# Kernel tuning notes

Measured on AMD Instinct MI355X. Metric: run time of the kernel, lower is better.

Reference implementation:

```python
import jax, jax.numpy as jnp
import numpy as np
from jax.scipy.special import logsumexp

TEMPERATURE = 0.1
BETA = 0.999
EPS = 1e-8
HARD_K = 10  # min(num_classes // 4, 10) with num_classes = 1000


def _l2norm(x, axis=-1):
    return x * jax.lax.rsqrt(jnp.sum(x * x, axis=axis, keepdims=True) + 1e-24)


def setup_inputs() -> dict:
    key = jax.random.key(0)
    k1, k2, k3, k4, k5 = jax.random.split(key, 5)
    B, D, C, M = 4096, 1024, 1000, 32768
    return {
        "image_features": jax.random.normal(k1, (B, D), dtype=jnp.float32),
        "prompts": jax.random.normal(k2, (C, D), dtype=jnp.float32),
        "labels": jax.random.randint(k3, (B, C), 0, 2, dtype=jnp.int32),
        "memory_features": jax.random.normal(k4, (M, D), dtype=jnp.float32),
        "memory_labels": jax.random.randint(k5, (M, C), 0, 2, dtype=jnp.int32),
        "mem_ptr": 16384,
    }


def reference(image_features, prompts, labels, memory_features, memory_labels, mem_ptr):
    B, D = image_features.shape
    C = prompts.shape[0]
    labels_f = labels.astype(jnp.float32)

    # z_img = F.normalize(image_features)
    z_img = _l2norm(image_features, axis=1)

    # class weights (effective-number reweighting), computed from this batch's labels
    counts = labels_f.sum(axis=0)                              # [C]
    effective_num = 1.0 - jnp.power(jnp.float32(BETA), counts)
    weights = (1.0 - BETA) / (effective_num + EPS)
    weights = weights / jnp.sum(weights) * C                   # [C]

    # memory bank update (detached write of current batch at ptr), then use [:ptr+B]
    mem_f = memory_features.at[mem_ptr:mem_ptr + B].set(jax.lax.stop_gradient(z_img))
    mem_l = memory_labels.at[mem_ptr:mem_ptr + B].set(labels)
    used = mem_ptr + B  # static

    enhanced_features = jnp.concatenate([z_img, mem_f[:used]], axis=0)     # [N, D]
    enhanced_labels = jnp.concatenate([labels_f, mem_l[:used].astype(jnp.float32)], axis=0)  # [N, C]

    z_prompts = _l2norm(prompts, axis=1)                       # [C, D]
    sim = (enhanced_features @ z_prompts.T) / TEMPERATURE      # [N, C]

    pos_mask = enhanced_labels > 0                             # [N, C]

    # hard negatives: top-K similarities among negatives define the keep threshold
    sim_for_neg = jnp.where(pos_mask, -jnp.inf, sim)
    hard_neg_vals, _ = jax.lax.top_k(sim_for_neg, HARD_K)      # [N, K]
    min_hard_neg = hard_neg_vals[:, -1:]                       # [N, 1]
    neg_mask = (~pos_mask) & (sim >= min_hard_neg)
    full_mask = pos_mask | neg_mask

    lse = logsumexp(jnp.where(full_mask, sim, -jnp.inf), axis=1)  # [N]
    log_prob = sim - lse[:, None]                              # [N, C]

    posf = pos_mask.astype(sim.dtype)
    pos_w = posf * weights[None, :]                            # [N, C]
    weight_sums = pos_w.sum(axis=1)                            # [N]
    loss_num = (pos_w * (-log_prob)).sum(axis=1)               # [N]

    valid = weight_sums > 0
    loss_per_sample = jnp.where(valid, loss_num / (weight_sums + EPS), 0.0)
    n_valid = jnp.maximum(valid.sum(), 1)
    attr_loss = loss_per_sample.sum() / n_valid.astype(sim.dtype)
    # single attribute -> total_loss / num_valid_attrs == attr_loss
    return attr_loss
```

## Files before the change

kernel.cpp:

```cpp
#include <hip/hip_runtime.h>
#include <math.h>

#define BN    4096
#define DD    1024
#define CC    1000
#define MM    32768
#define ROWS_CAP 32768


#define NGROUP_A 512
#define NGROUP_B 16
#define NCOUNT   512
#define NBITS    512

#define NSUB 16

typedef __attribute__((ext_vector_type(8))) int   int8v;
typedef __attribute__((ext_vector_type(16))) float f32x16;

__device__ __forceinline__ float wave_sum_f(float v) {
#pragma unroll
  for (int off = 32; off >= 1; off >>= 1) v += __shfl_xor(v, off, 64);
  return v;
}

__device__ __forceinline__ int pack4(float a, float b, float c, float d) {
  int p = __builtin_amdgcn_cvt_pk_fp8_f32(a, b, 0, false);
  p = __builtin_amdgcn_cvt_pk_fp8_f32(c, d, p, true);
  return p;
}

__device__ __forceinline__ void gload16(const unsigned char* g, unsigned char* l) {
  __builtin_amdgcn_global_load_lds(
      (const __attribute__((address_space(1))) unsigned int*)g,
      (__attribute__((address_space(3))) unsigned int*)l, 16, 0, 0);
}

__device__ __forceinline__ void ins10(float* t, float v) {
#pragma unroll
  for (int i = 9; i >= 1; --i) t[i] = __builtin_amdgcn_fmed3f(v, t[i - 1], t[i]);
  t[0] = fmaxf(t[0], v);
}

__global__ __launch_bounds__(256) void conv_kernel(const float* __restrict__ img,
                                                   const float* __restrict__ prompts,
                                                   const float* __restrict__ mem,
                                                   const int* __restrict__ memptr,
                                                   unsigned char* __restrict__ A,
                                                   unsigned char* __restrict__ B,
                                                   const int* __restrict__ labels,
                                                   const int* __restrict__ mlabels,
                                                   int* __restrict__ counts,
                                                   unsigned* __restrict__ bitmask) {
  const int blk = blockIdx.x;
  const int t = threadIdx.x;
  const int lane = t & 63;
  const int wid = t >> 6;
  const int nrows = BN + memptr[0];
  const int padded = (nrows + 127) & ~127;

  if (blk >= NGROUP_A + NGROUP_B + NCOUNT) {
    const int bi = blk - (NGROUP_A + NGROUP_B + NCOUNT);
    const int rowBase = bi * 64;
    if (rowBase >= padded) return;
    for (int i = 0; i < 16; ++i) {
      const int row = rowBase + wid * 16 + i;
      if (row >= padded) continue;
      unsigned bits = 0;
      if (row < nrows) {
        const int* lr = (row < BN) ? labels + (size_t)row * CC
                                   : mlabels + (size_t)(row - BN) * CC;
        const int cbase = lane * 16;
#pragma unroll
        for (int g = 0; g < 4; ++g) {
          int c = cbase + g * 4;
          int4 l4;
          if (c + 3 < CC) l4 = *(const int4*)(lr + c);
          else {
            l4.x = (c < CC) ? lr[c] : 0;
            l4.y = (c + 1 < CC) ? lr[c + 1] : 0;
            l4.z = (c + 2 < CC) ? lr[c + 2] : 0;
            l4.w = (c + 3 < CC) ? lr[c + 3] : 0;
          }
          unsigned m = 0;
          if (l4.x > 0) m |= 1u;
          if (l4.y > 0) m |= 2u;
          if (l4.z > 0) m |= 4u;
          if (l4.w > 0) m |= 8u;
          bits |= m << (g * 4);
        }
      }
      unsigned pair = __shfl_xor(bits, 1, 64);
      if (!(lane & 1)) bitmask[(size_t)row * 32 + (lane >> 1)] = bits | (pair << 16);
    }
    return;
  }

  if (blk >= NGROUP_A + NGROUP_B) {
    const int ci = blk - (NGROUP_A + NGROUP_B);
    const int c = (ci & 3) * 256 + t;
    if (c >= CC) return;
    const int b0 = (ci >> 2) * 32;
    int s = 0;
#pragma unroll
    for (int b = 0; b < 32; ++b) s += labels[(size_t)(b0 + b) * CC + c];
    atomicAdd(&counts[c], s);
    return;
  }

  __shared__ unsigned char tile[65536];

  const bool isB = (blk >= NGROUP_A);
  const int g = isB ? (blk - NGROUP_A) : blk;
  const int rowBase = g * 64;
  if (!isB && rowBase >= padded) return;

  unsigned char* dstBase = (isB ? B : A)
      + (size_t)(rowBase >> 7) * 131072 + (size_t)(rowBase & 64) * 16;

  for (int i = 0; i < 16; ++i) {
    const int r = wid * 16 + i;
    const int row = rowBase + r;
    const float* src = nullptr;
    float esc = 1.0f;
    bool needNorm = false;
    if (isB) {
      if (row < CC) { src = prompts + (size_t)row * DD; needNorm = true; esc = 10.0f; }
    } else {
      if (row < BN)         { src = img + (size_t)row * DD; needNorm = true; }
      else if (row < nrows) { src = mem + (size_t)(row - BN) * DD; }
    }
    int4 o = {0, 0, 0, 0};
    if (src) {
      const float4* s4 = (const float4*)src + lane * 4;
      float4 a = s4[0], b = s4[1], c = s4[2], d = s4[3];
      float sc = esc;
      if (needNorm) {
        float ss = a.x * a.x + a.y * a.y + a.z * a.z + a.w * a.w
                 + b.x * b.x + b.y * b.y + b.z * b.z + b.w * b.w
                 + c.x * c.x + c.y * c.y + c.z * c.z + c.w * c.w
                 + d.x * d.x + d.y * d.y + d.z * d.z + d.w * d.w;
        ss = wave_sum_f(ss);
        sc = esc * rsqrtf(ss + 1e-24f);
      }
      o.x = pack4(a.x * sc, a.y * sc, a.z * sc, a.w * sc);
      o.y = pack4(b.x * sc, b.y * sc, b.z * sc, b.w * sc);
      o.z = pack4(c.x * sc, c.y * sc, c.z * sc, c.w * sc);
      o.w = pack4(d.x * sc, d.y * sc, d.z * sc, d.w * sc);
    }
    *(int4*)(tile + lane * 1024 + (((r + lane) & 63) << 4)) = o;
  }
  __syncthreads();

#pragma unroll
  for (int p = 0; p < 16; ++p) {
    const int ochunk = p * 256 + t;
    const int kc = ochunk >> 6;
    const int rl = ochunk & 63;
    int4 v = *(const int4*)(tile + kc * 1024 + (((rl + kc) & 63) << 4));
    *(int4*)(dstBase + (size_t)kc * 2048 + rl * 16) = v;
  }
}

__global__ __launch_bounds__(512) void gemm_fused(
    const unsigned char* __restrict__ A, const unsigned char* __restrict__ Bm,
    const unsigned* __restrict__ bitmask, const int* __restrict__ counts,
    const int* __restrict__ memptr, float* __restrict__ partials) {
  const int f = blockIdx.x;
  const int x = f & 7;
  const int s = f >> 3;
  const int cb = s & 7;
  const int rt = (s >> 3) * 8 + x;

  const int nrows = BN + memptr[0];
  const int row0 = rt * 128;
  if (row0 >= nrows) return;
  const int c0 = cb * 128;

  __shared__ unsigned char As[2][16384];
  __shared__ unsigned char Bs[2][16384];
  __shared__ unsigned posbits[128][4];
  __shared__ float wcol[128];
  __shared__ float wpart[8];

  const int t = threadIdx.x;
  const int lane = t & 63;
  const int wid = t >> 6;
  const int wm = (wid >> 1) * 32;
  const int wn = (wid & 1) * 64;
  const int q = lane >> 5;
  const int rr = lane & 31;

  const unsigned char* gaT = A + (size_t)row0 * DD;
  const unsigned char* gbT = Bm + (size_t)c0 * DD;

#pragma unroll
  for (int p = 0; p < 2; ++p) {
    gload16(gaT + p * 8192 + t * 16, As[0] + p * 8192 + t * 16);
    gload16(gbT + p * 8192 + t * 16, Bs[0] + p * 8192 + t * 16);
  }
#pragma unroll
  for (int p = 0; p < 2; ++p) {
    gload16(gaT + 16384 + p * 8192 + t * 16, As[1] + p * 8192 + t * 16);
    gload16(gbT + 16384 + p * 8192 + t * 16, Bs[1] + p * 8192 + t * 16);
  }

  {
    float wv[2];
    float accw = 0.f;
#pragma unroll
    for (int i = 0; i < 2; ++i) {
      int c = t + i * 512;
      float w = 0.f;
      if (c < CC) {
        float cnt = (float)counts[c];
        float en = 1.0f - expf(cnt * logf(0.999f));
        w = (1.0f - 0.999f) / (en + 1e-8f);
      }
      wv[i] = w;
      accw += w;
    }
    float sw = wave_sum_f(accw);
    if (lane == 0) wpart[wid] = sw;
    if (t < 128) {
      const int4 bm = *(const int4*)(bitmask + (size_t)(row0 + t) * 32 + cb * 4);
      posbits[t][0] = bm.x; posbits[t][1] = bm.y;
      posbits[t][2] = bm.z; posbits[t][3] = bm.w;
    }
    __syncthreads();
    float tot = 0.f;
#pragma unroll
    for (int i = 0; i < 8; ++i) tot += wpart[i];
    float scw = (float)CC / tot;
#pragma unroll
    for (int i = 0; i < 2; ++i) {
      int c = t + i * 512;
      if (c >= c0 && c < c0 + 128) wcol[c - c0] = wv[i] * scw;
    }
  }

  f32x16 acc[2] = {};

  int cur = 0;
  for (int it = 0; it < 8; ++it) {
    if (it == 7) asm volatile("s_waitcnt vmcnt(0)" ::: "memory");
    else         asm volatile("s_waitcnt vmcnt(4)" ::: "memory");
    __builtin_amdgcn_sched_barrier(0);
    __builtin_amdgcn_s_barrier();
    __builtin_amdgcn_sched_barrier(0);
#pragma unroll
    for (int h = 0; h < 2; ++h) {
      const int kc = h * 4 + q * 2;
      int8v af, bfv[2];
      {
        const unsigned char* pa = As[cur] + kc * 2048 + (wm + rr) * 16;
        int4 lo4 = *(const int4*)pa;
        int4 hi4 = *(const int4*)(pa + 2048);
        af[0] = lo4.x; af[1] = lo4.y; af[2] = lo4.z; af[3] = lo4.w;
        af[4] = hi4.x; af[5] = hi4.y; af[6] = hi4.z; af[7] = hi4.w;
      }
#pragma unroll
      for (int ni = 0; ni < 2; ++ni) {
        const unsigned char* pb = Bs[cur] + kc * 2048 + (wn + ni * 32 + rr) * 16;
        int4 lo4 = *(const int4*)pb;
        int4 hi4 = *(const int4*)(pb + 2048);
        bfv[ni][0] = lo4.x; bfv[ni][1] = lo4.y; bfv[ni][2] = lo4.z; bfv[ni][3] = lo4.w;
        bfv[ni][4] = hi4.x; bfv[ni][5] = hi4.y; bfv[ni][6] = hi4.z; bfv[ni][7] = hi4.w;
      }
#pragma unroll
      for (int ni = 0; ni < 2; ++ni)
        acc[ni] = __builtin_amdgcn_mfma_scale_f32_32x32x64_f8f6f4(
            bfv[ni], af, acc[ni], 0, 0, 0, 127, 0, 127);
    }
    __builtin_amdgcn_sched_barrier(0);
    __builtin_amdgcn_s_barrier();
    __builtin_amdgcn_sched_barrier(0);
    if (it + 2 < 8) {
      const size_t kb = (size_t)(it + 2) * 16384;
#pragma unroll
      for (int p = 0; p < 2; ++p) {
        gload16(gaT + kb + p * 8192 + t * 16, As[cur] + p * 8192 + t * 16);
        gload16(gbT + kb + p * 8192 + t * 16, Bs[cur] + p * 8192 + t * 16);
      }
    }
    cur ^= 1;
  }

  const int cl = lane & 31;
  const int rl = wm + cl;
  const int row_g = row0 + rl;
  const int wnb = wid & 1;

  float t10[10];
#pragma unroll
  for (int i = 0; i < 10; ++i) t10[i] = -INFINITY;
  float m = -INFINITY, ssum = 0.f, wsum = 0.f, wsim = 0.f;
#pragma unroll
  for (int ni = 0; ni < 2; ++ni) {
    const unsigned bits = posbits[rl][wnb * 2 + ni];
    f32x16 v = acc[ni];
    float pq = -INFINITY;
    unsigned pb = 0;
#pragma unroll
    for (int reg = 0; reg < 16; ++reg) {
      const int ci = (reg & 3) + 8 * (reg >> 2) + 4 * q;
      const int cg = c0 + wn + ni * 32 + ci;
      const float val = v[reg];
      const bool cvalid = (cg < CC);
      const bool pos = cvalid && ((bits >> ci) & 1u);
      if (pos) {
        float w = wcol[wn + ni * 32 + ci];
        wsum += w;
        wsim += w * val;
        pq = fmaxf(pq, val);
        pb |= 1u << reg;
      }
      ins10(t10, (cvalid && !pos) ? val : -INFINITY);
    }
    if (pb) {
      float ps = 0.f;
#pragma unroll
      for (int reg = 0; reg < 16; ++reg)
        ps += expf(((pb >> reg) & 1u) ? (v[reg] - pq) : -INFINITY);
      float m2 = fmaxf(m, pq);
      ssum = ssum * expf(m - m2) + ps * expf(pq - m2);
      m = m2;
    }
  }

  {
    float o10[10];
#pragma unroll
    for (int j = 0; j < 10; ++j) o10[j] = __shfl_xor(t10[j], 32, 64);
#pragma unroll
    for (int j = 0; j < 10; ++j) ins10(t10, o10[j]);
    float pm2 = __shfl_xor(m, 32, 64);
    float ps2 = __shfl_xor(ssum, 32, 64);
    float w2  = __shfl_xor(wsum, 32, 64);
    float ws2 = __shfl_xor(wsim, 32, 64);
    if (ps2 > 0.f) {
      float m2 = fmaxf(m, pm2);
      ssum = ssum * expf(m - m2) + ps2 * expf(pm2 - m2);
      m = m2;
    }
    wsum += w2;
    wsim += ws2;
  }

  if (q == 0) {
    const int sub = cb * 2 + wnb;
    float* pp = partials + (size_t)sub * ROWS_CAP + row_g;
#pragma unroll
    for (int k = 0; k < 10; ++k) pp[(size_t)k * NSUB * ROWS_CAP] = t10[k];
    pp[(size_t)10 * NSUB * ROWS_CAP] = m;
    pp[(size_t)11 * NSUB * ROWS_CAP] = ssum;
    pp[(size_t)12 * NSUB * ROWS_CAP] = wsum;
    pp[(size_t)13 * NSUB * ROWS_CAP] = wsim;
  }
}

__global__ __launch_bounds__(256) void merge_kernel(const float* __restrict__ partials,
                                                    const int* __restrict__ memptr,
                                                    float* __restrict__ blk_lps,
                                                    float* __restrict__ blk_val) {
  const int t = threadIdx.x;
  const int row = blockIdx.x * 256 + t;
  const int nrows = BN + memptr[0];

  float cl = 0.f, cv = 0.f;
  if (row < nrows) {
    float t10[10];
#pragma unroll
    for (int i = 0; i < 10; ++i) t10[i] = -INFINITY;
    float Mp = -INFINITY, psum = 0.f, wsum = 0.f, wsim = 0.f;
    for (int sub = 0; sub < NSUB; ++sub) {
      const float* pp = partials + (size_t)sub * ROWS_CAP + row;
#pragma unroll
      for (int j = 0; j < 10; ++j) ins10(t10, pp[(size_t)j * NSUB * ROWS_CAP]);
      float pm = pp[(size_t)10 * NSUB * ROWS_CAP];
      float ps = pp[(size_t)11 * NSUB * ROWS_CAP];
      wsum += pp[(size_t)12 * NSUB * ROWS_CAP];
      wsim += pp[(size_t)13 * NSUB * ROWS_CAP];
      if (ps > 0.f) {
        float m2 = fmaxf(Mp, pm);
        psum = psum * expf(Mp - m2) + ps * expf(pm - m2);
        Mp = m2;
      }
    }
    const float M = fmaxf(Mp, t10[0]);
    float esum = 0.f;
#pragma unroll
    for (int j = 0; j < 10; ++j) esum += expf(t10[j] - M);
    if (psum > 0.f) esum += psum * expf(Mp - M);
    const float lse = M + logf(esum);
    const bool valid = (wsum > 0.f);
    const float lps = valid ? (wsum * lse - wsim) / (wsum + 1e-8f) : 0.f;
    const float mult = (row < BN) ? 2.f : 1.f;
    cl = mult * lps;
    cv = valid ? mult : 0.f;
  }
  cl = wave_sum_f(cl);
  cv = wave_sum_f(cv);
  __shared__ float p1[4], p2[4];
  if ((t & 63) == 0) { p1[t >> 6] = cl; p2[t >> 6] = cv; }
  __syncthreads();
  if (t == 0) {
    blk_lps[blockIdx.x] = p1[0] + p1[1] + p1[2] + p1[3];
    blk_val[blockIdx.x] = p2[0] + p2[1] + p2[2] + p2[3];
  }
}

__global__ __launch_bounds__(128) void reduce_kernel(const float* __restrict__ blk_lps,
                                                     const float* __restrict__ blk_val,
                                                     float* __restrict__ out) {
  const int t = threadIdx.x;
  float a = wave_sum_f(blk_lps[t]);
  float b = wave_sum_f(blk_val[t]);
  __shared__ float p1[2], p2[2];
  if ((t & 63) == 0) { p1[t >> 6] = a; p2[t >> 6] = b; }
  __syncthreads();
  if (t == 0) out[0] = (p1[0] + p1[1]) / fmaxf(p2[0] + p2[1], 1.0f);
}

extern "C" void kernel_launch(void* const* d_in, const int* in_sizes, int n_in,
                              void* d_out, int out_size, void* d_ws, size_t ws_size,
                              hipStream_t stream) {
  const float* img     = (const float*)d_in[0];
  const float* prompts = (const float*)d_in[1];
  const int*   labels  = (const int*)d_in[2];
  const float* mem     = (const float*)d_in[3];
  const int*   mlabels = (const int*)d_in[4];
  const int*   memptr  = (const int*)d_in[5];
  float* out = (float*)d_out;
  char* ws = (char*)d_ws;

  int*      counts  = (int*)(ws + 0);
  float*    blk_lps = (float*)(ws + 8192);
  float*    blk_val = (float*)(ws + 12288);
  unsigned* bitmask = (unsigned*)(ws + 270336);
  unsigned char* Bf8 = (unsigned char*)(ws + 4464640);
  unsigned char* Af8 = (unsigned char*)(ws + 5513216);
  float* partials = (float*)(ws + 5513216 + (size_t)ROWS_CAP * DD);

  hipMemsetAsync(ws, 0, 4096, stream);

  conv_kernel<<<NGROUP_A + NGROUP_B + NCOUNT + NBITS, 256, 0, stream>>>(
      img, prompts, mem, memptr, Af8, Bf8, labels, mlabels, counts, bitmask);

  gemm_fused<<<8 * (ROWS_CAP / 128), 512, 0, stream>>>(
      Af8, Bf8, bitmask, counts, memptr, partials);

  merge_kernel<<<ROWS_CAP / 256, 256, 0, stream>>>(partials, memptr, blk_lps, blk_val);

  reduce_kernel<<<1, 128, 0, stream>>>(blk_lps, blk_val, out);
}
```

Before: 397.7 us.

## Load GEMM A operand straight to registers and widen conversion blocks to 512 threads

The GEMM kernel no longer stages the A tile in LDS. Each wave loads its A fragments from global memory into registers and prefetches the next k-step, while B keeps a double-buffered LDS prefetch that now runs one step ahead, with a single __syncthreads per iteration. This cuts LDS traffic and shared-memory footprint, aiming for better occupancy or less LDS contention. In exchange, waves that share the same A rows load them redundantly, and the barrier's memory wait may limit how much the loads overlap with compute. The conversion, label-count and bitmask kernels are also regridded to 512-thread blocks with fewer rows per wave and unrolled loops.

```diff
diff --git a/kernel.cpp b/kernel.cpp
--- a/kernel.cpp
+++ b/kernel.cpp
@@ -8,10 +8,10 @@
 #define ROWS_CAP 32768
 
 
-#define NGROUP_A 512
-#define NGROUP_B 16
-#define NCOUNT   512
-#define NBITS    512
+#define NGA   512
+#define NGB   16
+#define NCNT  128
+#define NBIT  1024
 
 #define NSUB 16
 
@@ -42,7 +42,7 @@
   t[0] = fmaxf(t[0], v);
 }
 
-__global__ __launch_bounds__(256) void conv_kernel(const float* __restrict__ img,
+__global__ __launch_bounds__(512) void conv_kernel(const float* __restrict__ img,
                                                    const float* __restrict__ prompts,
                                                    const float* __restrict__ mem,
                                                    const int* __restrict__ memptr,
@@ -59,12 +59,13 @@
   const int nrows = BN + memptr[0];
   const int padded = (nrows + 127) & ~127;
 
-  if (blk >= NGROUP_A + NGROUP_B + NCOUNT) {
-    const int bi = blk - (NGROUP_A + NGROUP_B + NCOUNT);
-    const int rowBase = bi * 64;
+  if (blk >= NGA + NGB + NCNT) {
+    const int bi = blk - (NGA + NGB + NCNT);
+    const int rowBase = bi * 32;
     if (rowBase >= padded) return;
-    for (int i = 0; i < 16; ++i) {
-      const int row = rowBase + wid * 16 + i;
+#pragma unroll
+    for (int i = 0; i < 4; ++i) {
+      const int row = rowBase + wid * 4 + i;
       if (row >= padded) continue;
       unsigned bits = 0;
       if (row < nrows) {
@@ -96,30 +97,35 @@
     return;
   }
 
-  if (blk >= NGROUP_A + NGROUP_B) {
-    const int ci = blk - (NGROUP_A + NGROUP_B);
-    const int c = (ci & 3) * 256 + t;
-    if (c >= CC) return;
-    const int b0 = (ci >> 2) * 32;
-    int s = 0;
-#pragma unroll
-    for (int b = 0; b < 32; ++b) s += labels[(size_t)(b0 + b) * CC + c];
-    atomicAdd(&counts[c], s);
+  if (blk >= NGA + NGB) {
+    const int ci = blk - (NGA + NGB);
+    const int b0 = ci * 32;
+    int s1 = 0, s2 = 0;
+    const bool c2ok = (t + 512 < CC);
+#pragma unroll
+    for (int b = 0; b < 32; ++b) {
+      const int* lr = labels + (size_t)(b0 + b) * CC;
+      s1 += lr[t];
+      if (c2ok) s2 += lr[t + 512];
+    }
+    atomicAdd(&counts[t], s1);
+    if (c2ok) atomicAdd(&counts[t + 512], s2);
     return;
   }
 
   __shared__ unsigned char tile[65536];
 
-  const bool isB = (blk >= NGROUP_A);
-  const int g = isB ? (blk - NGROUP_A) : blk;
+  const bool isB = (blk >= NGA);
+  const int g = isB ? (blk - NGA) : blk;
   const int rowBase = g * 64;
   if (!isB && rowBase >= padded) return;
 
   unsigned char* dstBase = (isB ? B : A)
       + (size_t)(rowBase >> 7) * 131072 + (size_t)(rowBase & 64) * 16;
 
-  for (int i = 0; i < 16; ++i) {
-    const int r = wid * 16 + i;
+#pragma unroll
+  for (int i = 0; i < 8; ++i) {
+    const int r = wid * 8 + i;
     const int row = rowBase + r;
     const float* src = nullptr;
     float esc = 1.0f;
@@ -153,8 +159,8 @@
   __syncthreads();
 
 #pragma unroll
-  for (int p = 0; p < 16; ++p) {
-    const int ochunk = p * 256 + t;
+  for (int p = 0; p < 8; ++p) {
+    const int ochunk = p * 512 + t;
     const int kc = ochunk >> 6;
     const int rl = ochunk & 63;
     int4 v = *(const int4*)(tile + kc * 1024 + (((rl + kc) & 63) << 4));
@@ -177,7 +183,6 @@
   if (row0 >= nrows) return;
   const int c0 = cb * 128;
 
-  __shared__ unsigned char As[2][16384];
   __shared__ unsigned char Bs[2][16384];
   __shared__ unsigned posbits[128][4];
   __shared__ float wcol[128];
@@ -193,17 +198,18 @@
 
   const unsigned char* gaT = A + (size_t)row0 * DD;
   const unsigned char* gbT = Bm + (size_t)c0 * DD;
-
-#pragma unroll
-  for (int p = 0; p < 2; ++p) {
-    gload16(gaT + p * 8192 + t * 16, As[0] + p * 8192 + t * 16);
+  const unsigned char* aBase = gaT + (size_t)(q * 2) * 2048 + (size_t)(wm + rr) * 16;
+
+#pragma unroll
+  for (int p = 0; p < 2; ++p)
     gload16(gbT + p * 8192 + t * 16, Bs[0] + p * 8192 + t * 16);
-  }
-#pragma unroll
-  for (int p = 0; p < 2; ++p) {
-    gload16(gaT + 16384 + p * 8192 + t * 16, As[1] + p * 8192 + t * 16);
-    gload16(gbT + 16384 + p * 8192 + t * 16, Bs[1] + p * 8192 + t * 16);
-  }
+  int4 afc[4], afn[4];
+  afc[0] = *(const int4*)(aBase);
+  afc[1] = *(const int4*)(aBase + 2048);
+  afc[2] = *(const int4*)(aBase + 8192);
+  afc[3] = *(const int4*)(aBase + 8192 + 2048);
+#pragma unroll
+  for (int i = 0; i < 4; ++i) afn[i] = afc[i];
 
   {
     float wv[2];
@@ -243,46 +249,39 @@
 
   int cur = 0;
   for (int it = 0; it < 8; ++it) {
-    if (it == 7) asm volatile("s_waitcnt vmcnt(0)" ::: "memory");
-    else         asm volatile("s_waitcnt vmcnt(4)" ::: "memory");
-    __builtin_amdgcn_sched_barrier(0);
-    __builtin_amdgcn_s_barrier();
-    __builtin_amdgcn_sched_barrier(0);
+    if (it < 7) {
+      const size_t kb = (size_t)(it + 1) * 16384;
+#pragma unroll
+      for (int p = 0; p < 2; ++p)
+        gload16(gbT + kb + p * 8192 + t * 16, Bs[cur ^ 1] + p * 8192 + t * 16);
+      const unsigned char* an = aBase + kb;
+      afn[0] = *(const int4*)(an);
+      afn[1] = *(const int4*)(an + 2048);
+      afn[2] = *(const int4*)(an + 8192);
+      afn[3] = *(const int4*)(an + 8192 + 2048);
+    }
 #pragma unroll
     for (int h = 0; h < 2; ++h) {
       const int kc = h * 4 + q * 2;
-      int8v af, bfv[2];
-      {
-        const unsigned char* pa = As[cur] + kc * 2048 + (wm + rr) * 16;
-        int4 lo4 = *(const int4*)pa;
-        int4 hi4 = *(const int4*)(pa + 2048);
-        af[0] = lo4.x; af[1] = lo4.y; af[2] = lo4.z; af[3] = lo4.w;
-        af[4] = hi4.x; af[5] = hi4.y; af[6] = hi4.z; af[7] = hi4.w;
-      }
+      int8v a, bfv;
+      a[0] = afc[h * 2].x;     a[1] = afc[h * 2].y;
+      a[2] = afc[h * 2].z;     a[3] = afc[h * 2].w;
+      a[4] = afc[h * 2 + 1].x; a[5] = afc[h * 2 + 1].y;
+      a[6] = afc[h * 2 + 1].z; a[7] = afc[h * 2 + 1].w;
 #pragma unroll
       for (int ni = 0; ni < 2; ++ni) {
         const unsigned char* pb = Bs[cur] + kc * 2048 + (wn + ni * 32 + rr) * 16;
         int4 lo4 = *(const int4*)pb;
         int4 hi4 = *(const int4*)(pb + 2048);
-        bfv[ni][0] = lo4.x; bfv[ni][1] = lo4.y; bfv[ni][2] = lo4.z; bfv[ni][3] = lo4.w;
-        bfv[ni][4] = hi4.x; bfv[ni][5] = hi4.y; bfv[ni][6] = hi4.z; bfv[ni][7] = hi4.w;
-      }
-#pragma unroll
-      for (int ni = 0; ni < 2; ++ni)
+        bfv[0] = lo4.x; bfv[1] = lo4.y; bfv[2] = lo4.z; bfv[3] = lo4.w;
+        bfv[4] = hi4.x; bfv[5] = hi4.y; bfv[6] = hi4.z; bfv[7] = hi4.w;
         acc[ni] = __builtin_amdgcn_mfma_scale_f32_32x32x64_f8f6f4(
-            bfv[ni], af, acc[ni], 0, 0, 0, 127, 0, 127);
-    }
-    __builtin_amdgcn_sched_barrier(0);
-    __builtin_amdgcn_s_barrier();
-    __builtin_amdgcn_sched_barrier(0);
-    if (it + 2 < 8) {
-      const size_t kb = (size_t)(it + 2) * 16384;
-#pragma unroll
-      for (int p = 0; p < 2; ++p) {
-        gload16(gaT + kb + p * 8192 + t * 16, As[cur] + p * 8192 + t * 16);
-        gload16(gbT + kb + p * 8192 + t * 16, Bs[cur] + p * 8192 + t * 16);
-      }
-    }
+            bfv, a, acc[ni], 0, 0, 0, 127, 0, 127);
+      }
+    }
+    __syncthreads();
+#pragma unroll
+    for (int i = 0; i < 4; ++i) afc[i] = afn[i];
     cur ^= 1;
   }
 
@@ -444,7 +443,7 @@
 
   hipMemsetAsync(ws, 0, 4096, stream);
 
-  conv_kernel<<<NGROUP_A + NGROUP_B + NCOUNT + NBITS, 256, 0, stream>>>(
+  conv_kernel<<<NGA + NGB + NCNT + NBIT, 512, 0, stream>>>(
       img, prompts, mem, memptr, Af8, Bf8, labels, mlabels, counts, bitmask);
 
   gemm_fused<<<8 * (ROWS_CAP / 128), 512, 0, stream>>>(
```

After: 396.7 us. About the same (-0.3%).
